# Optimization experiments

Hardware: AMD Instinct MI355X
Metric: run time of the kernel (lower is better)

## Reference

```python
import jax, jax.numpy as jnp
import numpy as np

N_NODES = 50000
N_EDGES = 800000
IN_DIM = 128
OUT_DIM = 128


def setup_inputs() -> dict:
    key = jax.random.key(0)
    k1, k2, k3, k4, k5, k6 = jax.random.split(key, 6)
    X = jax.random.normal(k1, (N_NODES, IN_DIM), dtype=jnp.float32)
    src = jax.random.randint(k2, (N_EDGES,), 0, N_NODES, dtype=jnp.int32)
    dst = jax.random.randint(k3, (N_EDGES,), 0, N_NODES, dtype=jnp.int32)
    # nn.Linear(in, out, bias=False) weight has shape (out, in)
    lim = 1.0 / np.sqrt(IN_DIM)
    W_self = jax.random.uniform(k4, (OUT_DIM, IN_DIM), dtype=jnp.float32, minval=-lim, maxval=lim)
    W_neigh = jax.random.uniform(k5, (OUT_DIM, IN_DIM), dtype=jnp.float32, minval=-lim, maxval=lim)
    bias = jnp.zeros((OUT_DIM,), dtype=jnp.float32)
    return {"X": X, "src": src, "dst": dst, "W_self": W_self, "W_neigh": W_neigh, "bias": bias}


def reference(X, src, dst, W_self, W_neigh, bias):
    # h_u = ReLU( W_self x_u + sum_{(v->u) in E} W_neigh x_v + bias )
    # Transform once per node (n_nodes x in_dim x out_dim GEMMs), then
    # gather transformed source features and scatter-add into destinations.
    h_self = jnp.einsum('ni,oi->no', X, W_self)        # [N, out]
    xw_neigh = jnp.einsum('ni,oi->no', X, W_neigh)     # [N, out]
    h_neigh = jax.ops.segment_sum(xw_neigh[src], dst, num_segments=N_NODES)
    return jax.nn.relu(h_self + h_neigh + bias)
```

## Files before the change

kernel.cpp:

```cpp
#include <hip/hip_runtime.h>

#define IN_DIM 128
#define OUT_DIM 128
#define BM 64
#define KT 32

typedef __attribute__((ext_vector_type(8))) short short8v;
typedef __attribute__((ext_vector_type(4))) float float4v;

__device__ __forceinline__ unsigned short bf16_hi(float x) {
    unsigned int u = __float_as_uint(x);
    return (unsigned short)((u + 0x7fffu + ((u >> 16) & 1u)) >> 16);
}
__device__ __forceinline__ float bf16_tof(unsigned short h) {
    return __uint_as_float(((unsigned int)h) << 16);
}

__global__ void scatter_kernel(const float* __restrict__ X,
                               const int* __restrict__ src,
                               const int* __restrict__ dst,
                               float* __restrict__ A,
                               int n_edges) {
    int gtid = blockIdx.x * blockDim.x + threadIdx.x;
    int e = gtid >> 5;
    if (e >= n_edges) return;
    int sub = gtid & 31;
    int s = src[e];
    int d = dst[e];
    const float4 v = *reinterpret_cast<const float4*>(
        X + (size_t)s * IN_DIM + sub * 4);
    float* o = A + (size_t)d * IN_DIM + sub * 4;
    unsafeAtomicAdd(o + 0, v.x);
    unsafeAtomicAdd(o + 1, v.y);
    unsafeAtomicAdd(o + 2, v.z);
    unsafeAtomicAdd(o + 3, v.w);
}

__global__ void hist_kernel(const int* __restrict__ dst, int* __restrict__ counts,
                            int n_edges) {
    int i = blockIdx.x * blockDim.x + threadIdx.x;
    int e0 = i * 4;
    if (e0 + 4 <= n_edges) {
        int4 d4 = *reinterpret_cast<const int4*>(dst + e0);
        atomicAdd(&counts[d4.x], 1);
        atomicAdd(&counts[d4.y], 1);
        atomicAdd(&counts[d4.z], 1);
        atomicAdd(&counts[d4.w], 1);
    } else {
        for (int e = e0; e < n_edges; ++e) atomicAdd(&counts[dst[e]], 1);
    }
}

__global__ __launch_bounds__(256)
void scan1_kernel(const int* __restrict__ counts, int* __restrict__ offs,
                  int* __restrict__ bsums, int n) {
    __shared__ int tmp[256];
    const int tid = threadIdx.x;
    const int i = blockIdx.x * 256 + tid;
    const int v = (i < n) ? counts[i] : 0;
    tmp[tid] = v;
    __syncthreads();
    #pragma unroll
    for (int d = 1; d < 256; d <<= 1) {
        int t = (tid >= d) ? tmp[tid - d] : 0;
        __syncthreads();
        tmp[tid] += t;
        __syncthreads();
    }
    if (i < n) offs[i] = tmp[tid] - v;
    if (tid == 255) bsums[blockIdx.x] = tmp[255];
}

__global__ __launch_bounds__(256)
void scan2_kernel(int* __restrict__ bsums, int nb) {
    __shared__ int tmp[256];
    __shared__ int carry;
    const int tid = threadIdx.x;
    if (tid == 0) carry = 0;
    __syncthreads();
    for (int base = 0; base < nb; base += 256) {
        const int i = base + tid;
        const int v = (i < nb) ? bsums[i] : 0;
        tmp[tid] = v;
        __syncthreads();
        #pragma unroll
        for (int d = 1; d < 256; d <<= 1) {
            int t = (tid >= d) ? tmp[tid - d] : 0;
            __syncthreads();
            tmp[tid] += t;
            __syncthreads();
        }
        if (i < nb) bsums[i] = carry + tmp[tid] - v;
        __syncthreads();
        if (tid == 0) carry += tmp[255];
        __syncthreads();
    }
}

__global__ __launch_bounds__(256)
void scan3_kernel(int* __restrict__ offs, const int* __restrict__ bsums,
                  int* __restrict__ cursor, int n) {
    const int i = blockIdx.x * 256 + threadIdx.x;
    if (i < n) {
        const int o = offs[i] + bsums[blockIdx.x];
        offs[i] = o;
        cursor[i] = o;
    }
}

__global__ void bucket_kernel(const int* __restrict__ src,
                              const int* __restrict__ dst,
                              int* __restrict__ cursor,
                              int* __restrict__ src_sorted, int n_edges) {
    int e = blockIdx.x * blockDim.x + threadIdx.x;
    if (e < n_edges) {
        const int pos = atomicAdd(&cursor[dst[e]], 1);
        src_sorted[pos] = src[e];
    }
}

__global__ __launch_bounds__(256)
void accum_split_kernel(const float* __restrict__ X,
                        const int* __restrict__ offs,
                        const int* __restrict__ src_sorted,
                        unsigned short* __restrict__ Ahi,
                        unsigned short* __restrict__ Alo,
                        int n_nodes, int n_edges) {
    const int tid = threadIdx.x;
    const int u = blockIdx.x * 8 + (tid >> 5);
    if (u >= n_nodes) return;
    const int sub = tid & 31;

    const int beg = offs[u];
    const int end = (u == n_nodes - 1) ? n_edges : offs[u + 1];

    float4 acc = make_float4(0.f, 0.f, 0.f, 0.f);
    int e = beg;
    for (; e + 4 <= end; e += 4) {
        const int s0 = src_sorted[e + 0];
        const int s1 = src_sorted[e + 1];
        const int s2 = src_sorted[e + 2];
        const int s3 = src_sorted[e + 3];
        const float4 v0 = *reinterpret_cast<const float4*>(X + (size_t)s0 * IN_DIM + sub * 4);
        const float4 v1 = *reinterpret_cast<const float4*>(X + (size_t)s1 * IN_DIM + sub * 4);
        const float4 v2 = *reinterpret_cast<const float4*>(X + (size_t)s2 * IN_DIM + sub * 4);
        const float4 v3 = *reinterpret_cast<const float4*>(X + (size_t)s3 * IN_DIM + sub * 4);
        acc.x += v0.x + v1.x + v2.x + v3.x;
        acc.y += v0.y + v1.y + v2.y + v3.y;
        acc.z += v0.z + v1.z + v2.z + v3.z;
        acc.w += v0.w + v1.w + v2.w + v3.w;
    }
    for (; e < end; ++e) {
        const int s = src_sorted[e];
        const float4 v = *reinterpret_cast<const float4*>(X + (size_t)s * IN_DIM + sub * 4);
        acc.x += v.x; acc.y += v.y; acc.z += v.z; acc.w += v.w;
    }

    ushort4 hi, lo;
    hi.x = bf16_hi(acc.x); lo.x = bf16_hi(acc.x - bf16_tof(hi.x));
    hi.y = bf16_hi(acc.y); lo.y = bf16_hi(acc.y - bf16_tof(hi.y));
    hi.z = bf16_hi(acc.z); lo.z = bf16_hi(acc.z - bf16_tof(hi.z));
    hi.w = bf16_hi(acc.w); lo.w = bf16_hi(acc.w - bf16_tof(hi.w));
    *reinterpret_cast<ushort4*>(Ahi + (size_t)u * IN_DIM + sub * 4) = hi;
    *reinterpret_cast<ushort4*>(Alo + (size_t)u * IN_DIM + sub * 4) = lo;
}

__global__ void xsplit_kernel(const float* __restrict__ X,
                              unsigned short* __restrict__ Xsp, int n_nodes) {
    int i = blockIdx.x * blockDim.x + threadIdx.x;
    if (i >= n_nodes * 32) return;
    const int node = i >> 5, g = i & 31;
    const float4 x = *reinterpret_cast<const float4*>(X + (size_t)node * IN_DIM + g * 4);
    ushort4 hi, lo;
    hi.x = bf16_hi(x.x); lo.x = bf16_hi(x.x - bf16_tof(hi.x));
    hi.y = bf16_hi(x.y); lo.y = bf16_hi(x.y - bf16_tof(hi.y));
    hi.z = bf16_hi(x.z); lo.z = bf16_hi(x.z - bf16_tof(hi.z));
    hi.w = bf16_hi(x.w); lo.w = bf16_hi(x.w - bf16_tof(hi.w));
    *reinterpret_cast<ushort4*>(Xsp + (size_t)node * 256 + g * 4) = hi;
    *reinterpret_cast<ushort4*>(Xsp + (size_t)node * 256 + 128 + g * 4) = lo;
}

__global__ void wsplit_kernel(const float* __restrict__ W1,
                              const float* __restrict__ W2,
                              unsigned short* __restrict__ W1h,
                              unsigned short* __restrict__ W1l,
                              unsigned short* __restrict__ W2h,
                              unsigned short* __restrict__ W2l) {
    int i = blockIdx.x * blockDim.x + threadIdx.x;
    if (i >= OUT_DIM * IN_DIM) return;
    float a = W1[i], b = W2[i];
    unsigned short ah = bf16_hi(a), bh = bf16_hi(b);
    W1h[i] = ah; W1l[i] = bf16_hi(a - bf16_tof(ah));
    W2h[i] = bh; W2l[i] = bf16_hi(b - bf16_tof(bh));
}

__global__ __launch_bounds__(256, 4)
void mfma_gemm_kernel(const unsigned short* Xsp,
                      const unsigned short* __restrict__ Ahi,
                      const unsigned short* __restrict__ Alo,
                      const unsigned short* __restrict__ W1h,
                      const unsigned short* __restrict__ W1l,
                      const unsigned short* __restrict__ W2h,
                      const unsigned short* __restrict__ W2l,
                      const float* __restrict__ bias,
                      float* out,
                      int n_nodes) {
    __shared__ unsigned short Fs[64 * 64];
    __shared__ unsigned short Ws[128 * 64];

    const int tid  = threadIdx.x;
    const int lane = tid & 63;
    const int wid  = tid >> 6;
    const int wm   = wid >> 1;
    const int wn   = wid & 1;
    const int lr   = lane & 15;
    const int lk   = lane >> 4;
    const int node0 = blockIdx.x * 64;

    const int fr = tid >> 3;
    const int c  = tid & 7;
    const int swz = (c ^ (fr & 7)) * 8;

    float4v acc[2][4];
    #pragma unroll
    for (int mi = 0; mi < 2; ++mi)
        #pragma unroll
        for (int ni = 0; ni < 4; ++ni) acc[mi][ni] = (float4v)0.f;

    const unsigned short* wseg[6] = {W1h, W1l, W1h, W2h, W2l, W2h};

    short8v fv[2], wv[4];

    {
        const int khalf = 0;
        #pragma unroll
        for (int j = 0; j < 2; ++j) {
            const int node = node0 + fr + j * 32;
            short8v v = (short8v)0;
            if (node < n_nodes)
                v = *reinterpret_cast<const short8v*>(
                    Xsp + (size_t)node * 256 + khalf + c * 8);
            fv[j] = v;
        }
        #pragma unroll
        for (int j = 0; j < 4; ++j)
            wv[j] = *reinterpret_cast<const short8v*>(
                wseg[0] + (size_t)(fr + j * 32) * 128 + khalf + c * 8);
    }

    #pragma unroll
    for (int t = 0; t < 12; ++t) {
        __syncthreads();
        #pragma unroll
        for (int j = 0; j < 2; ++j)
            *reinterpret_cast<short8v*>(&Fs[(fr + j * 32) * 64 + swz]) = fv[j];
        #pragma unroll
        for (int j = 0; j < 4; ++j)
            *reinterpret_cast<short8v*>(&Ws[(fr + j * 32) * 64 + swz]) = wv[j];
        __syncthreads();

        if (t < 11) {
            const int tn = t + 1;
            const int seg = tn >> 1;
            const int khalf = (tn & 1) * 64;
            #pragma unroll
            for (int j = 0; j < 2; ++j) {
                const int node = node0 + fr + j * 32;
                short8v v = (short8v)0;
                if (node < n_nodes) {
                    if (seg < 3) {
                        v = *reinterpret_cast<const short8v*>(
                            Xsp + (size_t)node * 256 + (seg == 2 ? 128 : 0) +
                            khalf + c * 8);
                    } else {
                        const unsigned short* Ap = (seg == 5) ? Alo : Ahi;
                        v = *reinterpret_cast<const short8v*>(
                            Ap + (size_t)node * 128 + khalf + c * 8);
                    }
                }
                fv[j] = v;
            }
            #pragma unroll
            for (int j = 0; j < 4; ++j)
                wv[j] = *reinterpret_cast<const short8v*>(
                    wseg[seg] + (size_t)(fr + j * 32) * 128 + khalf + c * 8);
        }

        #pragma unroll
        for (int ks = 0; ks < 2; ++ks) {
            const int cc = ((ks * 4 + lk) ^ (lr & 7)) * 8;
            short8v a[2], b[4];
            #pragma unroll
            for (int mi = 0; mi < 2; ++mi) {
                const int row = wm * 32 + mi * 16 + lr;
                a[mi] = *reinterpret_cast<const short8v*>(&Fs[row * 64 + cc]);
            }
            #pragma unroll
            for (int ni = 0; ni < 4; ++ni) {
                const int o = wn * 64 + ni * 16 + lr;
                b[ni] = *reinterpret_cast<const short8v*>(&Ws[o * 64 + cc]);
            }
            #pragma unroll
            for (int mi = 0; mi < 2; ++mi)
                #pragma unroll
                for (int ni = 0; ni < 4; ++ni)
                    acc[mi][ni] = __builtin_amdgcn_mfma_f32_16x16x32_bf16(
                        a[mi], b[ni], acc[mi][ni], 0, 0, 0);
        }
    }

    #pragma unroll
    for (int ni = 0; ni < 4; ++ni) {
        const int o = wn * 64 + ni * 16 + lr;
        const float bo = bias[o];
        #pragma unroll
        for (int mi = 0; mi < 2; ++mi) {
            const int nodeb = node0 + wm * 32 + mi * 16 + lk * 4;
            #pragma unroll
            for (int r = 0; r < 4; ++r) {
                const int node = nodeb + r;
                if (node < n_nodes)
                    out[(size_t)node * OUT_DIM + o] =
                        fmaxf(acc[mi][ni][r] + bo, 0.f);
            }
        }
    }
}

__global__ __launch_bounds__(256)
void gemm_kernel(const float* __restrict__ X,
                 const float* __restrict__ A,
                 const float* __restrict__ Wself,
                 const float* __restrict__ Wneigh,
                 const float* __restrict__ bias,
                 float* __restrict__ out,
                 int n_nodes) {
    __shared__ alignas(16) float Wt[KT][132];
    __shared__ alignas(16) float Xs[BM][KT + 4];

    const int tid   = threadIdx.x;
    const int o_grp = tid & 31;
    const int n_grp = tid >> 5;
    const int node0 = blockIdx.x * BM;

    float acc[8][4];
    #pragma unroll
    for (int i = 0; i < 8; ++i)
        #pragma unroll
        for (int j = 0; j < 4; ++j) acc[i][j] = 0.f;

    for (int kt = 0; kt < 2 * IN_DIM; kt += KT) {
        const float* Wsrc = (kt < IN_DIM) ? Wself : Wneigh;
        const float* Fsrc = (kt < IN_DIM) ? X : A;
        const int kbase = kt & (IN_DIM - 1);
        __syncthreads();
        {
            const int k4 = tid & 7;
            int o = tid >> 3;
            #pragma unroll
            for (int p = 0; p < 4; ++p, o += 32) {
                float4 w = *reinterpret_cast<const float4*>(
                    Wsrc + o * IN_DIM + kbase + k4 * 4);
                Wt[k4 * 4 + 0][o] = w.x;
                Wt[k4 * 4 + 1][o] = w.y;
                Wt[k4 * 4 + 2][o] = w.z;
                Wt[k4 * 4 + 3][o] = w.w;
            }
        }
        {
            const int k4 = tid & 7;
            int n = tid >> 3;
            #pragma unroll
            for (int p = 0; p < 2; ++p, n += 32) {
                const int node = node0 + n;
                float4 x = make_float4(0.f, 0.f, 0.f, 0.f);
                if (node < n_nodes)
                    x = *reinterpret_cast<const float4*>(
                        Fsrc + (size_t)node * IN_DIM + kbase + k4 * 4);
                *reinterpret_cast<float4*>(&Xs[n][k4 * 4]) = x;
            }
        }
        __syncthreads();
        #pragma unroll
        for (int k4 = 0; k4 < KT; k4 += 4) {
            float4 w0 = *reinterpret_cast<const float4*>(&Wt[k4 + 0][o_grp * 4]);
            float4 w1 = *reinterpret_cast<const float4*>(&Wt[k4 + 1][o_grp * 4]);
            float4 w2 = *reinterpret_cast<const float4*>(&Wt[k4 + 2][o_grp * 4]);
            float4 w3 = *reinterpret_cast<const float4*>(&Wt[k4 + 3][o_grp * 4]);
            #pragma unroll
            for (int nn = 0; nn < 8; ++nn) {
                float4 x = *reinterpret_cast<const float4*>(
                    &Xs[n_grp * 8 + nn][k4]);
                acc[nn][0] = fmaf(x.x, w0.x, acc[nn][0]);
                acc[nn][0] = fmaf(x.y, w1.x, acc[nn][0]);
                acc[nn][0] = fmaf(x.z, w2.x, acc[nn][0]);
                acc[nn][0] = fmaf(x.w, w3.x, acc[nn][0]);
                acc[nn][1] = fmaf(x.x, w0.y, acc[nn][1]);
                acc[nn][1] = fmaf(x.y, w1.y, acc[nn][1]);
                acc[nn][1] = fmaf(x.z, w2.y, acc[nn][1]);
                acc[nn][1] = fmaf(x.w, w3.y, acc[nn][1]);
                acc[nn][2] = fmaf(x.x, w0.z, acc[nn][2]);
                acc[nn][2] = fmaf(x.y, w1.z, acc[nn][2]);
                acc[nn][2] = fmaf(x.z, w2.z, acc[nn][2]);
                acc[nn][2] = fmaf(x.w, w3.z, acc[nn][2]);
                acc[nn][3] = fmaf(x.x, w0.w, acc[nn][3]);
                acc[nn][3] = fmaf(x.y, w1.w, acc[nn][3]);
                acc[nn][3] = fmaf(x.z, w2.w, acc[nn][3]);
                acc[nn][3] = fmaf(x.w, w3.w, acc[nn][3]);
            }
        }
    }

    const float4 b = *reinterpret_cast<const float4*>(bias + o_grp * 4);
    #pragma unroll
    for (int nn = 0; nn < 8; ++nn) {
        const int node = node0 + n_grp * 8 + nn;
        if (node < n_nodes) {
            float4 r;
            r.x = fmaxf(acc[nn][0] + b.x, 0.f);
            r.y = fmaxf(acc[nn][1] + b.y, 0.f);
            r.z = fmaxf(acc[nn][2] + b.z, 0.f);
            r.w = fmaxf(acc[nn][3] + b.w, 0.f);
            *reinterpret_cast<float4*>(
                out + (size_t)node * OUT_DIM + o_grp * 4) = r;
        }
    }
}

extern "C" void kernel_launch(void* const* d_in, const int* in_sizes, int n_in,
                              void* d_out, int out_size, void* d_ws, size_t ws_size,
                              hipStream_t stream) {
    const float* X      = (const float*)d_in[0];
    const int*   src    = (const int*)d_in[1];
    const int*   dst    = (const int*)d_in[2];
    const float* Wself  = (const float*)d_in[3];
    const float* Wneigh = (const float*)d_in[4];
    const float* bias   = (const float*)d_in[5];
    float*       out    = (float*)d_out;

    const int n_nodes = in_sizes[0] / IN_DIM;
    const int n_edges = in_sizes[1];
    const int nb = (n_nodes + 255) / 256;

    char* w = (char*)d_ws;
    auto take = [&](size_t bytes) {
        char* p = w;
        w += (bytes + 15) & ~(size_t)15;
        return p;
    };
    unsigned short* Ahi = (unsigned short*)take((size_t)n_nodes * IN_DIM * 2);
    unsigned short* Alo = (unsigned short*)take((size_t)n_nodes * IN_DIM * 2);
    int* counts    = (int*)take((size_t)n_nodes * sizeof(int));
    int* offs      = (int*)take((size_t)n_nodes * sizeof(int));
    int* cursor    = (int*)take((size_t)n_nodes * sizeof(int));
    int* bsums     = (int*)take((size_t)nb * sizeof(int));
    int* srcsorted = (int*)take((size_t)n_edges * sizeof(int));
    unsigned short* W1h = (unsigned short*)take((size_t)OUT_DIM * IN_DIM * 2);
    unsigned short* W1l = (unsigned short*)take((size_t)OUT_DIM * IN_DIM * 2);
    unsigned short* W2h = (unsigned short*)take((size_t)OUT_DIM * IN_DIM * 2);
    unsigned short* W2l = (unsigned short*)take((size_t)OUT_DIM * IN_DIM * 2);
    const size_t needed = (size_t)(w - (char*)d_ws);

    const int eblocks = (n_edges + 255) / 256;

    if (needed <= ws_size) {
        hipMemsetAsync(counts, 0, (size_t)n_nodes * sizeof(int), stream);
        hist_kernel<<<(n_edges / 4 + 256) / 256 + 1, 256, 0, stream>>>(dst, counts, n_edges);
        scan1_kernel<<<nb, 256, 0, stream>>>(counts, offs, bsums, n_nodes);
        scan2_kernel<<<1, 256, 0, stream>>>(bsums, nb);
        scan3_kernel<<<nb, 256, 0, stream>>>(offs, bsums, cursor, n_nodes);
        bucket_kernel<<<eblocks, 256, 0, stream>>>(src, dst, cursor, srcsorted,
                                                   n_edges);
        unsigned short* Xsp = (unsigned short*)d_out;
        xsplit_kernel<<<(n_nodes * 32 + 255) / 256, 256, 0, stream>>>(X, Xsp, n_nodes);
        wsplit_kernel<<<(OUT_DIM * IN_DIM + 255) / 256, 256, 0, stream>>>(
            Wself, Wneigh, W1h, W1l, W2h, W2l);
        accum_split_kernel<<<(n_nodes + 7) / 8, 256, 0, stream>>>(
            X, offs, srcsorted, Ahi, Alo, n_nodes, n_edges);
        mfma_gemm_kernel<<<(n_nodes + 63) / 64, 256, 0, stream>>>(
            Xsp, Ahi, Alo, W1h, W1l, W2h, W2l, bias, out, n_nodes);
    } else {
        float* A = (float*)d_ws;
        hipMemsetAsync(A, 0, (size_t)n_nodes * IN_DIM * sizeof(float), stream);
        const long long sthreads = (long long)n_edges * 32;
        const int sblocks = (int)((sthreads + 255) / 256);
        scatter_kernel<<<sblocks, 256, 0, stream>>>(X, src, dst, A, n_edges);
        gemm_kernel<<<(n_nodes + BM - 1) / BM, 256, 0, stream>>>(
            X, A, Wself, Wneigh, bias, out, n_nodes);
    }
}
```

Baseline: 272.4 us.

## Partition bucket scatter by destination range across interleaved block groups

Replaces the one-thread-per-edge bucket kernel with a grid-stride kernel split into eight destination-range partitions. Consecutive blocks are assigned different partitions, so each group only issues atomics and writes for destinations in its slice, which is meant to keep cursor atomics and src_sorted writes within a smaller, more cache-resident address range. Edges are loaded as int4. In exchange, every partition re-reads the entire src and dst arrays, multiplying edge-list read traffic eightfold.

```diff
diff --git a/kernel.cpp b/kernel.cpp
--- a/kernel.cpp
+++ b/kernel.cpp
@@ -4,6 +4,7 @@
 #define OUT_DIM 128
 #define BM 64
 #define KT 32
+#define NPART 8
 
 typedef __attribute__((ext_vector_type(8))) short short8v;
 typedef __attribute__((ext_vector_type(4))) float float4v;
@@ -108,14 +109,36 @@
     }
 }
 
-__global__ void bucket_kernel(const int* __restrict__ src,
-                              const int* __restrict__ dst,
-                              int* __restrict__ cursor,
-                              int* __restrict__ src_sorted, int n_edges) {
-    int e = blockIdx.x * blockDim.x + threadIdx.x;
-    if (e < n_edges) {
-        const int pos = atomicAdd(&cursor[dst[e]], 1);
-        src_sorted[pos] = src[e];
+__global__ __launch_bounds__(256)
+void bucket_part_kernel(const int* __restrict__ src,
+                        const int* __restrict__ dst,
+                        int* __restrict__ cursor,
+                        int* __restrict__ src_sorted,
+                        int n_edges, int chunk) {
+    const int part = blockIdx.x & (NPART - 1);
+    const int lb   = blockIdx.x / NPART;
+    const int gt   = lb * 256 + threadIdx.x;
+    const int gstr = (gridDim.x / NPART) * 256;
+    const int lo = part * chunk;
+    const int hi = lo + chunk;
+
+    const int n4 = n_edges >> 2;
+    for (int i = gt; i < n4; i += gstr) {
+        const int4 d4 = reinterpret_cast<const int4*>(dst)[i];
+        const int4 s4 = reinterpret_cast<const int4*>(src)[i];
+        if (d4.x >= lo && d4.x < hi)
+            src_sorted[atomicAdd(&cursor[d4.x], 1)] = s4.x;
+        if (d4.y >= lo && d4.y < hi)
+            src_sorted[atomicAdd(&cursor[d4.y], 1)] = s4.y;
+        if (d4.z >= lo && d4.z < hi)
+            src_sorted[atomicAdd(&cursor[d4.z], 1)] = s4.z;
+        if (d4.w >= lo && d4.w < hi)
+            src_sorted[atomicAdd(&cursor[d4.w], 1)] = s4.w;
+    }
+    for (int e = (n4 << 2) + gt; e < n_edges; e += gstr) {
+        const int d = dst[e];
+        if (d >= lo && d < hi)
+            src_sorted[atomicAdd(&cursor[d], 1)] = src[e];
     }
 }
 
@@ -461,16 +484,15 @@
     unsigned short* W2l = (unsigned short*)take((size_t)OUT_DIM * IN_DIM * 2);
     const size_t needed = (size_t)(w - (char*)d_ws);
 
-    const int eblocks = (n_edges + 255) / 256;
-
     if (needed <= ws_size) {
         hipMemsetAsync(counts, 0, (size_t)n_nodes * sizeof(int), stream);
         hist_kernel<<<(n_edges / 4 + 256) / 256 + 1, 256, 0, stream>>>(dst, counts, n_edges);
         scan1_kernel<<<nb, 256, 0, stream>>>(counts, offs, bsums, n_nodes);
         scan2_kernel<<<1, 256, 0, stream>>>(bsums, nb);
         scan3_kernel<<<nb, 256, 0, stream>>>(offs, bsums, cursor, n_nodes);
-        bucket_kernel<<<eblocks, 256, 0, stream>>>(src, dst, cursor, srcsorted,
-                                                   n_edges);
+        const int chunk = (n_nodes + NPART - 1) / NPART;
+        bucket_part_kernel<<<2048, 256, 0, stream>>>(src, dst, cursor,
+                                                     srcsorted, n_edges, chunk);
         unsigned short* Xsp = (unsigned short*)d_out;
         xsplit_kernel<<<(n_nodes * 32 + 255) / 256, 256, 0, stream>>>(X, Xsp, n_nodes);
         wsplit_kernel<<<(OUT_DIM * IN_DIM + 255) / 256, 256, 0, stream>>>(
```

Result: faster. 263.7 us (-3.2%).
